# Optimization experiments

Measured on AMD Instinct MI355X. Metric: run time of the kernel, lower is better.

The kernel has to match this reference:

```python
import jax, jax.numpy as jnp
import numpy as np

N, F, D, K, B, L, E, H = 12288, 128, 128, 3, 64, 256, 393216, 8
DT = 2 * D  # token dim
ALPHA = 0.5


def _mlp(h, w1, b1, w2, b2):
    return jax.nn.relu(h @ w1 + b1) @ w2 + b2


def setup_inputs() -> dict:
    key = jax.random.key(0)
    ks = jax.random.split(key, 24)
    s = 0.05
    x = jax.random.normal(ks[0], (N, F), jnp.float32)
    proj_w = jax.random.normal(ks[1], (F, D), jnp.float32) * s
    proj_b = jnp.zeros((D,), jnp.float32)
    adj_rows = jax.random.randint(ks[2], (E,), 0, N, jnp.int32)
    adj_cols = jax.random.randint(ks[3], (E,), 0, N, jnp.int32)
    adj_vals = jax.random.uniform(ks[4], (E,), jnp.float32) / 32.0
    ppr = jax.random.uniform(ks[5], (N, N), jnp.float32) * 0.01
    drnl = jax.random.uniform(ks[6], (B, N), jnp.float32) * 10.0
    src = jax.random.randint(ks[7], (B,), 0, N, jnp.int32)
    dst = jax.random.randint(ks[8], (B,), 0, N, jnp.int32)
    sample_idx = jnp.repeat(jnp.arange(B, dtype=jnp.int32), L)
    node_idx = jax.random.randint(ks[9], (B, L), 0, N, jnp.int32)
    node_idx = node_idx.at[:, 0].set(src).at[:, 1].set(dst).reshape(-1)
    enc_w1 = jax.random.normal(ks[10], (4, 2, D), jnp.float32) * 0.2
    enc_b1 = jnp.zeros((4, D), jnp.float32)
    enc_w2 = jax.random.normal(ks[11], (4, D, D), jnp.float32) * s
    enc_b2 = jnp.zeros((4, D), jnp.float32)
    struct_w1 = jax.random.normal(ks[12], (4 * D, D), jnp.float32) * s
    struct_b1 = jnp.zeros((D,), jnp.float32)
    struct_w2 = jax.random.normal(ks[13], (D, D), jnp.float32) * s
    struct_b2 = jnp.zeros((D,), jnp.float32)
    cls_tok = jax.random.normal(ks[14], (DT,), jnp.float32) * s
    wq = jax.random.normal(ks[15], (DT, DT), jnp.float32) * s
    wk = jax.random.normal(ks[16], (DT, DT), jnp.float32) * s
    wv = jax.random.normal(ks[17], (DT, DT), jnp.float32) * s
    wo = jax.random.normal(ks[18], (DT, DT), jnp.float32) * s
    return dict(x=x, proj_w=proj_w, proj_b=proj_b, adj_vals=adj_vals,
                adj_rows=adj_rows, adj_cols=adj_cols, ppr=ppr, drnl=drnl,
                src=src, dst=dst, sample_idx=sample_idx, node_idx=node_idx,
                enc_w1=enc_w1, enc_b1=enc_b1, enc_w2=enc_w2, enc_b2=enc_b2,
                struct_w1=struct_w1, struct_b1=struct_b1, struct_w2=struct_w2,
                struct_b2=struct_b2, cls_tok=cls_tok, wq=wq, wk=wk, wv=wv, wo=wo)


def reference(x, proj_w, proj_b, adj_vals, adj_rows, adj_cols, ppr, drnl,
              src, dst, sample_idx, node_idx,
              enc_w1, enc_b1, enc_w2, enc_b2,
              struct_w1, struct_b1, struct_w2, struct_b2,
              cls_tok, wq, wk, wv, wo):
    # --- re_features: feature_proj + K sparse matmul hops, APPNP-style mix ---
    feats = x @ proj_w + proj_b                      # [N, D]
    h = feats
    for _ in range(K):
        h = jax.ops.segment_sum(adj_vals[:, None] * h[adj_cols], adj_rows,
                                num_segments=N)      # sparse adj @ h
    re_x = h * (1.0 - ALPHA) + feats * ALPHA         # [N, D]

    # --- cal_heuristic: dense ppr row gather + drnl lookup ---
    n = sample_idx.shape[0]
    ppr_a = ppr[src[sample_idx], node_idx]           # [n]
    ppr_b = ppr[dst[sample_idx], node_idx]
    drnl_v = drnl[sample_idx, node_idx]
    heur = jnp.zeros((n, 4, 2), jnp.float32)
    heur = heur.at[:, 2, 0].set(ppr_a).at[:, 2, 1].set(ppr_b)
    heur = heur.at[:, 3, 0].set(drnl_v).at[:, 3, 1].set(drnl_v)

    # --- tokenizer: 4 heuristic MLPs -> structure MLP, concat node feats ---
    enc = jax.vmap(_mlp)(heur.transpose(1, 0, 2), enc_w1, enc_b1, enc_w2, enc_b2)
    struct_in = enc.transpose(1, 0, 2).reshape(n, 4 * D)   # [n, 4D] (CN,AA,PPR,DRNL)
    struct = _mlp(struct_in, struct_w1, struct_b1, struct_w2, struct_b2)  # [n, D]
    tok = jnp.concatenate([struct, re_x[node_idx]], axis=-1).reshape(B, L, DT)

    # --- GraphTransformer: CLS + multi-head self-attention ---
    cls = jnp.broadcast_to(cls_tok, (B, 1, DT))
    seq = jnp.concatenate([cls, tok], axis=1)        # [B, L+1, DT]
    dh = DT // H
    q = (seq @ wq).reshape(B, L + 1, H, dh)
    k = (seq @ wk).reshape(B, L + 1, H, dh)
    v = (seq @ wv).reshape(B, L + 1, H, dh)
    att = jax.nn.softmax(jnp.einsum('bqhd,bkhd->bhqk', q, k) / jnp.sqrt(jnp.float32(dh)), axis=-1)
    out = jnp.einsum('bhqk,bkhd->bqhd', att, v).reshape(B, L + 1, DT) @ wo
    h_cls, h_a, h_b = out[:, 0], out[:, 1], out[:, 2]
    return jnp.concatenate([h_a, h_b, h_cls], axis=-1)  # [B, 6*dim]
```

## Files before the change

kernel.cpp:

```cpp
#include <hip/hip_runtime.h>
#include <math.h>

#define NN 12288
#define FD 128
#define DD 128
#define EE 393216
#define BB 64
#define LL 256
#define HH 8
#define DTD 256
#define NTOK 16384
#define CAP 128

#define PROJ_B0 1536
#define PREP_B0 1728
#define HEUR_B0 1796
#define SBIAS_B 1860
#define CLS_B   1861
#define SETUP_GRID 1862

#define SEQ_ST 272
#define STG_ST 272

typedef float f32x4 __attribute__((ext_vector_type(4)));
typedef short s16x8 __attribute__((ext_vector_type(8)));

__device__ __forceinline__ float relu_(float x){ return fmaxf(x, 0.0f); }

__device__ __forceinline__ unsigned short f2b(float f){
  unsigned int u = __float_as_uint(f);
  u += 0x7FFFu + ((u >> 16) & 1u);
  return (unsigned short)(u >> 16);
}
__device__ __forceinline__ float b2f(unsigned short h){
  return __uint_as_float(((unsigned int)h) << 16);
}

__device__ __forceinline__ f32x4 MF(s16x8 a, s16x8 b, f32x4 c){
  return __builtin_amdgcn_mfma_f32_16x16x32_bf16(a, b, c, 0, 0, 0);
}

__global__ void __launch_bounds__(256)
k_setup(const float* __restrict__ x, const float* __restrict__ proj_w,
        const float* __restrict__ proj_b, unsigned short* __restrict__ featsb,
        const float* __restrict__ wq, const float* __restrict__ wk,
        const float* __restrict__ wv,
        const float* __restrict__ enc_w2, const float* __restrict__ sw1,
        const float* __restrict__ sw2, const float* __restrict__ cls_tok,
        unsigned short* __restrict__ wqT, unsigned short* __restrict__ wkT,
        unsigned short* __restrict__ wvT,
        unsigned short* __restrict__ w2T2, unsigned short* __restrict__ w2T3,
        unsigned short* __restrict__ sw1aT, unsigned short* __restrict__ sw1bT,
        unsigned short* __restrict__ sw2T,
        const int* __restrict__ node_idx, const int* __restrict__ srcI,
        const int* __restrict__ dstI, const float* __restrict__ ppr,
        const float* __restrict__ drnl, float* __restrict__ heurA,
        float* __restrict__ heurB, float* __restrict__ heurD,
        const int* __restrict__ adj_rows, const int* __restrict__ adj_cols,
        const float* __restrict__ adj_vals, int* __restrict__ cnt,
        uint2* __restrict__ ccv,
        const float* __restrict__ enc_b1, const float* __restrict__ enc_b2,
        const float* __restrict__ sb1, float* __restrict__ sbias,
        float* __restrict__ qcls, unsigned short* __restrict__ kcls,
        unsigned short* __restrict__ vcls){
  int t = threadIdx.x;
  if(blockIdx.x < PROJ_B0){
    int e = blockIdx.x*256 + t;
    int r = adj_rows[e];
    int p = atomicAdd(&cnt[r], 1);
    ccv[(size_t)r*CAP + p] = make_uint2((unsigned)adj_cols[e], __float_as_uint(adj_vals[e]));
  } else if(blockIdx.x < PREP_B0){
    int bid = blockIdx.x - PROJ_B0;
    int row0 = bid * 64;
    int lane = t & 63, w = t >> 6;
    int lr = lane & 15, lg = lane >> 4;
    f32x4 acc[4][2];
    #pragma unroll
    for(int nt=0;nt<2;++nt){
      int col = w*32 + nt*16 + lr;
      float bv = proj_b[col];
      #pragma unroll
      for(int rt=0;rt<4;++rt)
        #pragma unroll
        for(int i=0;i<4;++i) acc[rt][nt][i]=bv;
    }
    #pragma unroll
    for(int ks=0; ks<4; ++ks){
      int kb = ks*32 + lg*8;
      s16x8 Bf[2];
      #pragma unroll
      for(int nt=0;nt<2;++nt){
        int col = w*32 + nt*16 + lr;
        #pragma unroll
        for(int i=0;i<8;++i) Bf[nt][i] = (short)f2b(proj_w[(kb+i)*DD + col]);
      }
      #pragma unroll
      for(int rt=0;rt<4;++rt){
        int row = row0 + rt*16 + lr;
        const f32x4* xp = (const f32x4*)(x + (size_t)row*FD + kb);
        f32x4 v0 = xp[0], v1 = xp[1];
        s16x8 Af;
        #pragma unroll
        for(int i=0;i<4;++i){ Af[i] = (short)f2b(v0[i]); Af[4+i] = (short)f2b(v1[i]); }
        #pragma unroll
        for(int nt=0;nt<2;++nt) acc[rt][nt] = MF(Af, Bf[nt], acc[rt][nt]);
      }
    }
    #pragma unroll
    for(int rt=0;rt<4;++rt)
      #pragma unroll
      for(int nt=0;nt<2;++nt)
        #pragma unroll
        for(int i=0;i<4;++i){
          int row = row0 + rt*16 + lg*4 + i;
          int col = w*32 + nt*16 + lr;
          featsb[(size_t)row*DD + col] = f2b(acc[rt][nt][i]);
        }
  } else if(blockIdx.x < HEUR_B0){
    int bid = blockIdx.x - PREP_B0;
    const float* s; unsigned short* d; int S, k0, n0;
    if(bid < 48){
      int m = bid >> 4, t16 = bid & 15;
      s = (m==0)? wq : (m==1)? wk : wv;
      d = (m==0)? wqT : (m==1)? wkT : wvT;
      S = 256; k0 = (t16>>2)*64; n0 = (t16&3)*64;
    } else {
      int b2 = bid - 48; int m = b2 >> 2, t4 = b2 & 3;
      if(m==0){ s = enc_w2 + 2*16384; d = w2T2; }
      else if(m==1){ s = enc_w2 + 3*16384; d = w2T3; }
      else if(m==2){ s = sw1 + 256*128; d = sw1aT; }
      else if(m==3){ s = sw1 + 384*128; d = sw1bT; }
      else { s = sw2; d = sw2T; }
      S = 128; k0 = (t4>>1)*64; n0 = (t4&1)*64;
    }
    __shared__ unsigned short tile[64][65];
    #pragma unroll
    for(int it=0; it<16; ++it){
      int idx = t + it*256;
      int i = idx>>6, j = idx&63;
      tile[i][j] = f2b(s[(size_t)(k0+i)*S + n0 + j]);
    }
    __syncthreads();
    #pragma unroll
    for(int it=0; it<16; ++it){
      int idx = t + it*256;
      int i2 = idx>>6, j2 = idx&63;
      d[(size_t)(n0+i2)*S + k0 + j2] = tile[j2][i2];
    }
  } else if(blockIdx.x < SBIAS_B){
    int tt = (blockIdx.x - HEUR_B0)*256 + t;
    int s = tt >> 8;
    int node = node_idx[tt];
    heurA[tt] = ppr[(size_t)srcI[s]*NN + node];
    heurB[tt] = ppr[(size_t)dstI[s]*NN + node];
    heurD[tt] = drnl[(size_t)s*NN + node];
  } else if(blockIdx.x == SBIAS_B){
    __shared__ float h0[DD], h1[DD], e0[DD], e1[DD];
    if(t < DD){
      h0[t] = relu_(enc_b1[0*DD+t]);
      h1[t] = relu_(enc_b1[1*DD+t]);
    }
    __syncthreads();
    if(t < DD){
      float a0 = enc_b2[0*DD+t], a1 = enc_b2[1*DD+t];
      for(int d2=0; d2<DD; ++d2){
        a0 += h0[d2]*enc_w2[(0*DD+d2)*DD + t];
        a1 += h1[d2]*enc_w2[(1*DD+d2)*DD + t];
      }
      e0[t]=a0; e1[t]=a1;
    }
    __syncthreads();
    if(t < DD){
      float sv = sb1[t];
      for(int d2=0; d2<DD; ++d2)
        sv += e0[d2]*sw1[d2*DD + t] + e1[d2]*sw1[(DD+d2)*DD + t];
      sbias[t]=sv;
    }
  } else {
    __shared__ float scls[DTD];
    scls[t] = cls_tok[t];
    __syncthreads();
    float aq=0.f, ak=0.f, av=0.f;
    for(int d2=0; d2<DTD; ++d2){
      float cv = scls[d2];
      aq += cv*wq[d2*DTD + t];
      ak += cv*wk[d2*DTD + t];
      av += cv*wv[d2*DTD + t];
    }
    qcls[t] = aq;
    kcls[t] = f2b(ak);
    vcls[t] = f2b(av);
  }
}

__global__ void __launch_bounds__(256)
k_spmm_w(const unsigned int* __restrict__ hin32, unsigned int* __restrict__ hout32,
         const int* __restrict__ cnt, const uint2* __restrict__ ccv,
         const unsigned int* __restrict__ featsb32, int finalpass){
  int lane = threadIdx.x & 63;
  int r = blockIdx.x*4 + (threadIdx.x>>6);
  int deg = cnt[r];
  const uint2* base = ccv + (size_t)r*CAP;
  float a0=0.f,a1=0.f,b0=0.f,b1=0.f,c0=0.f,c1=0.f,d0=0.f,d1=0.f;
  int p = 0;
  for(; p+4 <= deg; p += 4){
    uint2 q0 = base[p], q1 = base[p+1], q2 = base[p+2], q3 = base[p+3];
    unsigned u0 = hin32[(size_t)q0.x*64 + lane];
    unsigned u1 = hin32[(size_t)q1.x*64 + lane];
    unsigned u2 = hin32[(size_t)q2.x*64 + lane];
    unsigned u3 = hin32[(size_t)q3.x*64 + lane];
    float v0=__uint_as_float(q0.y), v1=__uint_as_float(q1.y);
    float v2=__uint_as_float(q2.y), v3=__uint_as_float(q3.y);
    a0 += v0*b2f((unsigned short)(u0&0xffffu)); a1 += v0*b2f((unsigned short)(u0>>16));
    b0 += v1*b2f((unsigned short)(u1&0xffffu)); b1 += v1*b2f((unsigned short)(u1>>16));
    c0 += v2*b2f((unsigned short)(u2&0xffffu)); c1 += v2*b2f((unsigned short)(u2>>16));
    d0 += v3*b2f((unsigned short)(u3&0xffffu)); d1 += v3*b2f((unsigned short)(u3>>16));
  }
  for(; p < deg; ++p){
    uint2 q0 = base[p];
    unsigned u0 = hin32[(size_t)q0.x*64 + lane];
    float v0 = __uint_as_float(q0.y);
    a0 += v0*b2f((unsigned short)(u0&0xffffu)); a1 += v0*b2f((unsigned short)(u0>>16));
  }
  a0 += b0 + c0 + d0;
  a1 += b1 + c1 + d1;
  if(finalpass){
    unsigned f = featsb32[(size_t)r*64 + lane];
    a0 = 0.5f*a0 + 0.5f*b2f((unsigned short)(f & 0xffffu));
    a1 = 0.5f*a1 + 0.5f*b2f((unsigned short)(f >> 16));
  }
  hout32[(size_t)r*64 + lane] = (unsigned)f2b(a0) | ((unsigned)f2b(a1) << 16);
}

__global__ void __launch_bounds__(512)
k_tok_kv(const int* __restrict__ node_idx,
         const float* __restrict__ heurA, const float* __restrict__ heurB,
         const float* __restrict__ heurD,
         const float* __restrict__ enc_w1, const float* __restrict__ enc_b1,
         const unsigned short* __restrict__ w2T2, const unsigned short* __restrict__ w2T3,
         const float* __restrict__ enc_b2,
         const unsigned short* __restrict__ sw1aT, const unsigned short* __restrict__ sw1bT,
         const float* __restrict__ sbias,
         const unsigned short* __restrict__ sw2T, const float* __restrict__ sb2,
         const unsigned short* __restrict__ rexb,
         const unsigned short* __restrict__ wkT, const unsigned short* __restrict__ wvT,
         const unsigned short* __restrict__ wqT,
         unsigned short* __restrict__ kbuf, unsigned short* __restrict__ vbuf,
         float* __restrict__ qbuf){
  __shared__ float sA[64], sB[64], sDV[64];
  __shared__ int sNode[64];
  __shared__ __align__(16) unsigned short hid[64*136];
  __shared__ __align__(16) unsigned short uni[64*STG_ST];
  unsigned short* pe2 = uni;
  unsigned short* pe3 = uni + 64*136;
  unsigned short* seq = uni;
  unsigned short* stg = uni;

  int tid = threadIdx.x;
  int lane = tid & 63;
  int w = tid >> 6;
  int lr = lane & 15;
  int lg = lane >> 4;
  int t0 = blockIdx.x * 64;
  int bs = t0 >> 8;
  int p0 = t0 & 255;

  if(tid < 64){
    int tt = t0 + tid;
    sNode[tid] = node_idx[tt];
    sA[tid]  = heurA[tt];
    sB[tid]  = heurB[tt];
    sDV[tid] = heurD[tt];
  }
  __syncthreads();

  int colm = w*16 + lr;

  {
    f32x4 acc2[4], acc3[4];
    float b2v = enc_b2[2*DD + colm];
    float b3v = enc_b2[3*DD + colm];
    #pragma unroll
    for(int rt=0;rt<4;++rt)
      #pragma unroll
      for(int i=0;i<4;++i){ acc2[rt][i]=b2v; acc3[rt][i]=b3v; }
    #pragma unroll
    for(int ks=0; ks<4; ++ks){
      int kb = ks*32 + lg*8;
      float w20[8], w21[8], w3s[8], b2c[8], b3c[8];
      #pragma unroll
      for(int i=0;i<8;++i){
        int k = kb + i;
        w20[i] = enc_w1[4*DD + k];
        w21[i] = enc_w1[5*DD + k];
        w3s[i] = enc_w1[6*DD + k] + enc_w1[7*DD + k];
        b2c[i] = enc_b1[2*DD + k];
        b3c[i] = enc_b1[3*DD + k];
      }
      s16x8 B2 = *(const s16x8*)(w2T2 + colm*DD + kb);
      s16x8 B3 = *(const s16x8*)(w2T3 + colm*DD + kb);
      #pragma unroll
      for(int rt=0;rt<4;++rt){
        int row = rt*16 + lr;
        float a = sA[row], b = sB[row], dv = sDV[row];
        s16x8 A2, A3;
        #pragma unroll
        for(int i=0;i<8;++i){
          A2[i] = (short)f2b(relu_(a*w20[i] + b*w21[i] + b2c[i]));
          A3[i] = (short)f2b(relu_(dv*w3s[i] + b3c[i]));
        }
        acc2[rt] = MF(A2, B2, acc2[rt]);
        acc3[rt] = MF(A3, B3, acc3[rt]);
      }
    }
    #pragma unroll
    for(int rt=0;rt<4;++rt)
      #pragma unroll
      for(int i=0;i<4;++i){
        int row = rt*16 + lg*4 + i;
        pe2[row*136 + colm] = f2b(acc2[rt][i]);
        pe3[row*136 + colm] = f2b(acc3[rt][i]);
      }
  }
  __syncthreads();

  {
    f32x4 acc[4];
    float sv = sbias[colm];
    #pragma unroll
    for(int rt=0;rt<4;++rt)
      #pragma unroll
      for(int i=0;i<4;++i) acc[rt][i]=sv;
    #pragma unroll
    for(int ks=0; ks<4; ++ks){
      int kb = ks*32 + lg*8;
      s16x8 Ba = *(const s16x8*)(sw1aT + colm*DD + kb);
      s16x8 Bb = *(const s16x8*)(sw1bT + colm*DD + kb);
      #pragma unroll
      for(int rt=0;rt<4;++rt){
        s16x8 A2 = *(const s16x8*)&pe2[(rt*16+lr)*136 + kb];
        s16x8 A3 = *(const s16x8*)&pe3[(rt*16+lr)*136 + kb];
        acc[rt] = MF(A2, Ba, acc[rt]);
        acc[rt] = MF(A3, Bb, acc[rt]);
      }
    }
    __syncthreads();
    #pragma unroll
    for(int rt=0;rt<4;++rt)
      #pragma unroll
      for(int i=0;i<4;++i){
        int row = rt*16 + lg*4 + i;
        hid[row*136 + colm] = f2b(relu_(acc[rt][i]));
      }
  }
  __syncthreads();

  {
    f32x4 acc[4];
    float bv = sb2[colm];
    #pragma unroll
    for(int rt=0;rt<4;++rt)
      #pragma unroll
      for(int i=0;i<4;++i) acc[rt][i]=bv;
    #pragma unroll
    for(int ks=0; ks<4; ++ks){
      int kb = ks*32 + lg*8;
      s16x8 Bc = *(const s16x8*)(sw2T + colm*DD + kb);
      #pragma unroll
      for(int rt=0;rt<4;++rt){
        s16x8 A = *(const s16x8*)&hid[(rt*16+lr)*136 + kb];
        acc[rt] = MF(A, Bc, acc[rt]);
      }
    }
    #pragma unroll
    for(int rt=0;rt<4;++rt)
      #pragma unroll
      for(int i=0;i<4;++i){
        int row = rt*16 + lg*4 + i;
        seq[row*SEQ_ST + colm] = f2b(acc[rt][i]);
      }
    int row = tid >> 3, c = (tid & 7)*16;
    int node = sNode[row];
    const unsigned short* rp = rexb + (size_t)node*DD + c;
    *(s16x8*)(seq + row*SEQ_ST + DD + c)     = *(const s16x8*)(rp);
    *(s16x8*)(seq + row*SEQ_ST + DD + c + 8) = *(const s16x8*)(rp + 8);
  }
  __syncthreads();

  f32x4 accK[4][2], accV[4][2];
  {
    #pragma unroll
    for(int rt=0;rt<4;++rt)
      #pragma unroll
      for(int nt=0;nt<2;++nt)
        #pragma unroll
        for(int i=0;i<4;++i){ accK[rt][nt][i]=0.f; accV[rt][nt][i]=0.f; }
    int col0 = w * 32;
    #pragma unroll
    for(int ks=0; ks<8; ++ks){
      int kb = ks*32 + lg*8;
      s16x8 A[4], Bk[2], Bv[2];
      #pragma unroll
      for(int rt=0;rt<4;++rt)
        A[rt] = *(const s16x8*)&seq[(rt*16+lr)*SEQ_ST + kb];
      #pragma unroll
      for(int nt=0;nt<2;++nt){
        int col = col0 + nt*16 + lr;
        Bk[nt] = *(const s16x8*)(wkT + (size_t)col*DTD + kb);
        Bv[nt] = *(const s16x8*)(wvT + (size_t)col*DTD + kb);
      }
      #pragma unroll
      for(int rt=0;rt<4;++rt)
        #pragma unroll
        for(int nt=0;nt<2;++nt){
          accK[rt][nt] = MF(A[rt], Bk[nt], accK[rt][nt]);
          accV[rt][nt] = MF(A[rt], Bv[nt], accV[rt][nt]);
        }
    }
  }
  if(p0 == 0){
    int qi = tid >> 8, col = tid & 255;
    float acc = 0.f;
    for(int d=0; d<DTD; d+=8){
      s16x8 wv8 = *(const s16x8*)(wqT + (size_t)col*DTD + d);
      #pragma unroll
      for(int j=0;j<8;++j)
        acc += b2f(seq[qi*SEQ_ST + d + j]) * b2f((unsigned short)wv8[j]);
    }
    qbuf[(size_t)(bs*2+qi)*DTD + col] = acc;
  }
  __syncthreads();

  {
    int col0 = w * 32;
    #pragma unroll
    for(int rt=0;rt<4;++rt)
      #pragma unroll
      for(int nt=0;nt<2;++nt)
        #pragma unroll
        for(int i=0;i<4;++i)
          stg[(rt*16 + lg*4 + i)*STG_ST + col0 + nt*16 + lr] = f2b(accK[rt][nt][i]);
  }
  __syncthreads();
  {
    int row = tid >> 3, c = (tid & 7)*32;
    #pragma unroll
    for(int j=0;j<4;++j)
      *(s16x8*)(kbuf + (size_t)(t0+row)*DTD + c + j*8) = *(const s16x8*)&stg[row*STG_ST + c + j*8];
  }
  __syncthreads();
  {
    int col0 = w * 32;
    #pragma unroll
    for(int rt=0;rt<4;++rt)
      #pragma unroll
      for(int nt=0;nt<2;++nt)
        #pragma unroll
        for(int i=0;i<4;++i)
          stg[(rt*16 + lg*4 + i)*STG_ST + col0 + nt*16 + lr] = f2b(accV[rt][nt][i]);
  }
  __syncthreads();
  {
    int row = tid >> 3, c = (tid & 7)*32;
    #pragma unroll
    for(int j=0;j<4;++j)
      *(s16x8*)(vbuf + (size_t)(t0+row)*DTD + c + j*8) = *(const s16x8*)&stg[row*STG_ST + c + j*8];
  }
}

__global__ void __launch_bounds__(256)
k_att2(const float* __restrict__ qcls, const float* __restrict__ qbuf,
       const unsigned short* __restrict__ kcls, const unsigned short* __restrict__ vcls,
       const unsigned short* __restrict__ kbuf, const unsigned short* __restrict__ vbuf,
       float* __restrict__ att_o){
  __shared__ float q_s[3][32];
  __shared__ float sc[3][257];
  __shared__ float ppv[8][3][32];
  int t = threadIdx.x;
  int b = blockIdx.x >> 3, h = blockIdx.x & 7;

  if(t < 96){
    int qi = t>>5, dd = t&31;
    q_s[qi][dd] = (qi==0) ? qcls[h*32 + dd]
                          : qbuf[(size_t)(b*2+qi-1)*DTD + h*32 + dd];
  }
  __syncthreads();
  const float scale = 0.17677669529663687f;
  for(int kk=t; kk<257; kk+=256){
    const unsigned short* kr = (kk==0) ? (kcls + h*32)
                                       : (kbuf + (size_t)(b*256+kk-1)*DTD + h*32);
    float kv[32];
    #pragma unroll
    for(int j=0;j<4;++j){
      s16x8 u = *(const s16x8*)(kr + j*8);
      #pragma unroll
      for(int m2=0;m2<8;++m2) kv[j*8+m2] = b2f((unsigned short)u[m2]);
    }
    float d0=0.f,d1=0.f,d2=0.f;
    #pragma unroll
    for(int dd=0;dd<32;++dd){
      d0 += q_s[0][dd]*kv[dd]; d1 += q_s[1][dd]*kv[dd]; d2 += q_s[2][dd]*kv[dd];
    }
    sc[0][kk]=d0*scale; sc[1][kk]=d1*scale; sc[2][kk]=d2*scale;
  }
  __syncthreads();
  {
    int wv = t>>6, lane = t&63;
    if(wv < 3){
      int qi = wv;
      float x0=sc[qi][lane], x1=sc[qi][lane+64], x2=sc[qi][lane+128], x3=sc[qi][lane+192];
      float x4 = (lane==0)? sc[qi][256] : -1e30f;
      float m = fmaxf(fmaxf(fmaxf(x0,x1),fmaxf(x2,x3)),x4);
      #pragma unroll
      for(int off=32; off>0; off>>=1) m = fmaxf(m, __shfl_xor(m, off));
      float e0=expf(x0-m), e1=expf(x1-m), e2v=expf(x2-m), e3v=expf(x3-m);
      float e4=(lane==0)? expf(x4-m) : 0.f;
      float s = e0+e1+e2v+e3v+e4;
      #pragma unroll
      for(int off=32; off>0; off>>=1) s += __shfl_xor(s, off);
      float inv = 1.0f/s;
      sc[qi][lane]=e0*inv; sc[qi][lane+64]=e1*inv;
      sc[qi][lane+128]=e2v*inv; sc[qi][lane+192]=e3v*inv;
      if(lane==0) sc[qi][256]=e4*inv;
    }
  }
  __syncthreads();
  {
    int dd = t & 31, g = t >> 5;
    float a0=0.f, a1=0.f, a2=0.f;
    for(int kk=g; kk<257; kk+=8){
      const unsigned short* vr = (kk==0) ? (vcls + h*32)
                                         : (vbuf + (size_t)(b*256+kk-1)*DTD + h*32);
      float v = b2f(vr[dd]);
      a0 += sc[0][kk]*v; a1 += sc[1][kk]*v; a2 += sc[2][kk]*v;
    }
    ppv[g][0][dd]=a0; ppv[g][1][dd]=a1; ppv[g][2][dd]=a2;
  }
  __syncthreads();
  if(t < 96){
    int qi = t>>5, dd = t&31;
    float s = 0.f;
    #pragma unroll
    for(int gg=0; gg<8; ++gg) s += ppv[gg][qi][dd];
    att_o[(size_t)(b*3+qi)*DTD + h*32 + dd] = s;
  }
}

__global__ void k_out(const float* __restrict__ att_o, const float* __restrict__ wo,
                      float* __restrict__ out){
  __shared__ float srow[DTD];
  int t = threadIdx.x;
  int r = blockIdx.x;
  int b = r/3, qi = r - b*3;
  srow[t] = att_o[(size_t)r*DTD + t];
  __syncthreads();
  float acc = 0.f;
  for(int d=0; d<DTD; ++d) acc += srow[d]*wo[d*DTD + t];
  int off = (qi==1)? 0 : ((qi==2)? DTD : 2*DTD);
  out[(size_t)b*768 + off + t] = acc;
}

extern "C" void kernel_launch(void* const* d_in, const int* in_sizes, int n_in,
                              void* d_out, int out_size, void* d_ws, size_t ws_size,
                              hipStream_t stream){
  const float* x        = (const float*)d_in[0];
  const float* proj_w   = (const float*)d_in[1];
  const float* proj_b   = (const float*)d_in[2];
  const float* adj_vals = (const float*)d_in[3];
  const int*   adj_rows = (const int*)d_in[4];
  const int*   adj_cols = (const int*)d_in[5];
  const float* ppr      = (const float*)d_in[6];
  const float* drnl     = (const float*)d_in[7];
  const int*   srcI     = (const int*)d_in[8];
  const int*   dstI     = (const int*)d_in[9];
  const int*   node_idx   = (const int*)d_in[11];
  const float* enc_w1   = (const float*)d_in[12];
  const float* enc_b1   = (const float*)d_in[13];
  const float* enc_w2   = (const float*)d_in[14];
  const float* enc_b2   = (const float*)d_in[15];
  const float* sw1      = (const float*)d_in[16];
  const float* sb1      = (const float*)d_in[17];
  const float* sw2      = (const float*)d_in[18];
  const float* sb2      = (const float*)d_in[19];
  const float* cls_tok  = (const float*)d_in[20];
  const float* wq       = (const float*)d_in[21];
  const float* wk       = (const float*)d_in[22];
  const float* wv       = (const float*)d_in[23];
  const float* wo       = (const float*)d_in[24];
  float* out = (float*)d_out;

  char* p = (char*)d_ws;
  auto alloc = [&](size_t bytes)->void*{ void* r = (void*)p; p += (bytes + 63) & ~(size_t)63; return r; };
  unsigned short* featsb = (unsigned short*)alloc((size_t)NN*DD*2);
  unsigned short* h1b    = (unsigned short*)alloc((size_t)NN*DD*2);
  unsigned short* h2b    = (unsigned short*)alloc((size_t)NN*DD*2);
  unsigned short* rexb   = (unsigned short*)alloc((size_t)NN*DD*2);
  int*   cnt     = (int*)  alloc((size_t)NN*4);
  uint2* ccv     = (uint2*)alloc((size_t)NN*CAP*8);
  float* sbias   = (float*)alloc((size_t)DD*4);
  float* heurA   = (float*)alloc((size_t)NTOK*4);
  float* heurB   = (float*)alloc((size_t)NTOK*4);
  float* heurD   = (float*)alloc((size_t)NTOK*4);
  unsigned short* kbuf = (unsigned short*)alloc((size_t)NTOK*DTD*2);
  unsigned short* vbuf = (unsigned short*)alloc((size_t)NTOK*DTD*2);
  float* qbuf    = (float*)alloc((size_t)BB*2*DTD*4);
  float* qcls    = (float*)alloc((size_t)DTD*4);
  unsigned short* kcls = (unsigned short*)alloc((size_t)DTD*2);
  unsigned short* vcls = (unsigned short*)alloc((size_t)DTD*2);
  float* att_o   = (float*)alloc((size_t)BB*3*DTD*4);
  unsigned short* wqT   = (unsigned short*)alloc((size_t)DTD*DTD*2);
  unsigned short* wkT   = (unsigned short*)alloc((size_t)DTD*DTD*2);
  unsigned short* wvT   = (unsigned short*)alloc((size_t)DTD*DTD*2);
  unsigned short* w2T2  = (unsigned short*)alloc((size_t)DD*DD*2);
  unsigned short* w2T3  = (unsigned short*)alloc((size_t)DD*DD*2);
  unsigned short* sw1aT = (unsigned short*)alloc((size_t)DD*DD*2);
  unsigned short* sw1bT = (unsigned short*)alloc((size_t)DD*DD*2);
  unsigned short* sw2T  = (unsigned short*)alloc((size_t)DD*DD*2);

  hipMemsetAsync(cnt, 0, NN*sizeof(int), stream);

  k_setup  <<<SETUP_GRID, 256, 0, stream>>>(x, proj_w, proj_b, featsb,
                                            wq, wk, wv, enc_w2, sw1, sw2, cls_tok,
                                            wqT, wkT, wvT, w2T2, w2T3, sw1aT, sw1bT, sw2T,
                                            node_idx, srcI, dstI, ppr, drnl,
                                            heurA, heurB, heurD,
                                            adj_rows, adj_cols, adj_vals, cnt, ccv,
                                            enc_b1, enc_b2, sb1, sbias,
                                            qcls, kcls, vcls);
  k_spmm_w <<<NN/4,   256, 0, stream>>>((const unsigned*)featsb, (unsigned*)h1b, cnt, ccv, (const unsigned*)featsb, 0);
  k_spmm_w <<<NN/4,   256, 0, stream>>>((const unsigned*)h1b, (unsigned*)h2b, cnt, ccv, (const unsigned*)featsb, 0);
  k_spmm_w <<<NN/4,   256, 0, stream>>>((const unsigned*)h2b, (unsigned*)rexb, cnt, ccv, (const unsigned*)featsb, 1);
  k_tok_kv <<<NTOK/64,512, 0, stream>>>(node_idx, heurA, heurB, heurD,
                                        enc_w1, enc_b1, w2T2, w2T3, enc_b2,
                                        sw1aT, sw1bT, sbias, sw2T, sb2, rexb,
                                        wkT, wvT, wqT, kbuf, vbuf, qbuf);
  k_att2   <<<BB*HH,  256, 0, stream>>>(qcls, qbuf, kcls, vcls, kbuf, vbuf, att_o);
  k_out    <<<BB*3,   256, 0, stream>>>(att_o, wo, out);
}
```

Before: 154.2 us.

## Fuse adjacency scatter and three SpMM passes into one cooperative kernel; fuse attention with output projection

Moves the adjacency bucketing out of the setup kernel and runs it, together with the counter zeroing and the three propagation passes, inside a single cooperative kernel that uses grid-wide syncs between phases. This replaces a memset and four separate launches. It also merges the per-head attention kernel and the output-projection kernel into one kernel per (batch, query) that handles all heads, removing the att_o round trip. Risks are grid-sync cost and lower occupancy with only 1024 persistent blocks on the SpMM phase, and fewer blocks (192) in the attention kernel. If the cooperative launch fails, the code falls back to separate kernels.

```diff
diff --git a/kernel.cpp b/kernel.cpp
--- a/kernel.cpp
+++ b/kernel.cpp
@@ -1,4 +1,5 @@
 #include <hip/hip_runtime.h>
+#include <hip/hip_cooperative_groups.h>
 #include <math.h>
 
 #define NN 12288
@@ -12,12 +13,14 @@
 #define NTOK 16384
 #define CAP 128
 
-#define PROJ_B0 1536
-#define PREP_B0 1728
-#define HEUR_B0 1796
-#define SBIAS_B 1860
-#define CLS_B   1861
-#define SETUP_GRID 1862
+#define PROJ_B0 0
+#define PREP_B0 192
+#define HEUR_B0 260
+#define SBIAS_B 324
+#define CLS_B   325
+#define SETUP_GRID 326
+
+#define COOP_BLOCKS 1024
 
 #define SEQ_ST 272
 #define STG_ST 272
@@ -38,6 +41,91 @@
 
 __device__ __forceinline__ f32x4 MF(s16x8 a, s16x8 b, f32x4 c){
   return __builtin_amdgcn_mfma_f32_16x16x32_bf16(a, b, c, 0, 0, 0);
+}
+
+__device__ __forceinline__ void spmm_row(int r, int lane,
+    const unsigned int* __restrict__ hin32, unsigned int* __restrict__ hout32,
+    const int* __restrict__ cnt, const uint2* __restrict__ ccv,
+    const unsigned int* __restrict__ featsb32, int finalpass){
+  int deg = cnt[r];
+  const uint2* base = ccv + (size_t)r*CAP;
+  float a0=0.f,a1=0.f,b0=0.f,b1=0.f,c0=0.f,c1=0.f,d0=0.f,d1=0.f;
+  int p = 0;
+  for(; p+4 <= deg; p += 4){
+    uint2 q0 = base[p], q1 = base[p+1], q2 = base[p+2], q3 = base[p+3];
+    unsigned u0 = hin32[(size_t)q0.x*64 + lane];
+    unsigned u1 = hin32[(size_t)q1.x*64 + lane];
+    unsigned u2 = hin32[(size_t)q2.x*64 + lane];
+    unsigned u3 = hin32[(size_t)q3.x*64 + lane];
+    float v0=__uint_as_float(q0.y), v1=__uint_as_float(q1.y);
+    float v2=__uint_as_float(q2.y), v3=__uint_as_float(q3.y);
+    a0 += v0*b2f((unsigned short)(u0&0xffffu)); a1 += v0*b2f((unsigned short)(u0>>16));
+    b0 += v1*b2f((unsigned short)(u1&0xffffu)); b1 += v1*b2f((unsigned short)(u1>>16));
+    c0 += v2*b2f((unsigned short)(u2&0xffffu)); c1 += v2*b2f((unsigned short)(u2>>16));
+    d0 += v3*b2f((unsigned short)(u3&0xffffu)); d1 += v3*b2f((unsigned short)(u3>>16));
+  }
+  for(; p < deg; ++p){
+    uint2 q0 = base[p];
+    unsigned u0 = hin32[(size_t)q0.x*64 + lane];
+    float v0 = __uint_as_float(q0.y);
+    a0 += v0*b2f((unsigned short)(u0&0xffffu)); a1 += v0*b2f((unsigned short)(u0>>16));
+  }
+  a0 += b0 + c0 + d0;
+  a1 += b1 + c1 + d1;
+  if(finalpass){
+    unsigned f = featsb32[(size_t)r*64 + lane];
+    a0 = 0.5f*a0 + 0.5f*b2f((unsigned short)(f & 0xffffu));
+    a1 = 0.5f*a1 + 0.5f*b2f((unsigned short)(f >> 16));
+  }
+  hout32[(size_t)r*64 + lane] = (unsigned)f2b(a0) | ((unsigned)f2b(a1) << 16);
+}
+
+__global__ void __launch_bounds__(256, 4)
+k_coop(unsigned short* __restrict__ featsb, unsigned short* __restrict__ h1b,
+       unsigned short* __restrict__ h2b, unsigned short* __restrict__ rexb,
+       int* __restrict__ cnt, uint2* __restrict__ ccv,
+       const int* __restrict__ adj_rows, const int* __restrict__ adj_cols,
+       const float* __restrict__ adj_vals){
+  cooperative_groups::grid_group gg = cooperative_groups::this_grid();
+  int t = threadIdx.x, bid = blockIdx.x;
+  int gid = bid*256 + t;
+  int lane = t & 63, wv = t >> 6;
+
+  if(gid < NN) cnt[gid] = 0;
+  gg.sync();
+
+  for(int e = gid; e < EE; e += COOP_BLOCKS*256){
+    int r = adj_rows[e];
+    int p = atomicAdd(&cnt[r], 1);
+    ccv[(size_t)r*CAP + p] = make_uint2((unsigned)adj_cols[e], __float_as_uint(adj_vals[e]));
+  }
+  gg.sync();
+
+  int r0 = bid*12 + wv*3;
+  #pragma unroll
+  for(int i=0;i<3;++i) spmm_row(r0+i, lane, (const unsigned*)featsb, (unsigned*)h1b, cnt, ccv, (const unsigned*)featsb, 0);
+  gg.sync();
+  #pragma unroll
+  for(int i=0;i<3;++i) spmm_row(r0+i, lane, (const unsigned*)h1b, (unsigned*)h2b, cnt, ccv, (const unsigned*)featsb, 0);
+  gg.sync();
+  #pragma unroll
+  for(int i=0;i<3;++i) spmm_row(r0+i, lane, (const unsigned*)h2b, (unsigned*)rexb, cnt, ccv, (const unsigned*)featsb, 1);
+}
+
+__global__ void k_scatter(const int* __restrict__ rows, const int* __restrict__ cols,
+                          const float* __restrict__ vals, int* __restrict__ cnt,
+                          uint2* __restrict__ ccv){
+  int e = blockIdx.x*256 + threadIdx.x;
+  int r = rows[e];
+  int p = atomicAdd(&cnt[r], 1);
+  ccv[(size_t)r*CAP + p] = make_uint2((unsigned)cols[e], __float_as_uint(vals[e]));
+}
+__global__ void __launch_bounds__(256)
+k_spmm_w(const unsigned int* __restrict__ hin32, unsigned int* __restrict__ hout32,
+         const int* __restrict__ cnt, const uint2* __restrict__ ccv,
+         const unsigned int* __restrict__ featsb32, int finalpass){
+  spmm_row(blockIdx.x*4 + (threadIdx.x>>6), threadIdx.x & 63,
+           hin32, hout32, cnt, ccv, featsb32, finalpass);
 }
 
 __global__ void __launch_bounds__(256)
@@ -56,20 +144,12 @@
         const int* __restrict__ dstI, const float* __restrict__ ppr,
         const float* __restrict__ drnl, float* __restrict__ heurA,
         float* __restrict__ heurB, float* __restrict__ heurD,
-        const int* __restrict__ adj_rows, const int* __restrict__ adj_cols,
-        const float* __restrict__ adj_vals, int* __restrict__ cnt,
-        uint2* __restrict__ ccv,
         const float* __restrict__ enc_b1, const float* __restrict__ enc_b2,
         const float* __restrict__ sb1, float* __restrict__ sbias,
         float* __restrict__ qcls, unsigned short* __restrict__ kcls,
         unsigned short* __restrict__ vcls){
   int t = threadIdx.x;
-  if(blockIdx.x < PROJ_B0){
-    int e = blockIdx.x*256 + t;
-    int r = adj_rows[e];
-    int p = atomicAdd(&cnt[r], 1);
-    ccv[(size_t)r*CAP + p] = make_uint2((unsigned)adj_cols[e], __float_as_uint(adj_vals[e]));
-  } else if(blockIdx.x < PREP_B0){
+  if(blockIdx.x < PREP_B0){
     int bid = blockIdx.x - PROJ_B0;
     int row0 = bid * 64;
     int lane = t & 63, w = t >> 6;
@@ -191,45 +271,6 @@
     kcls[t] = f2b(ak);
     vcls[t] = f2b(av);
   }
-}
-
-__global__ void __launch_bounds__(256)
-k_spmm_w(const unsigned int* __restrict__ hin32, unsigned int* __restrict__ hout32,
-         const int* __restrict__ cnt, const uint2* __restrict__ ccv,
-         const unsigned int* __restrict__ featsb32, int finalpass){
-  int lane = threadIdx.x & 63;
-  int r = blockIdx.x*4 + (threadIdx.x>>6);
-  int deg = cnt[r];
-  const uint2* base = ccv + (size_t)r*CAP;
-  float a0=0.f,a1=0.f,b0=0.f,b1=0.f,c0=0.f,c1=0.f,d0=0.f,d1=0.f;
-  int p = 0;
-  for(; p+4 <= deg; p += 4){
-    uint2 q0 = base[p], q1 = base[p+1], q2 = base[p+2], q3 = base[p+3];
-    unsigned u0 = hin32[(size_t)q0.x*64 + lane];
-    unsigned u1 = hin32[(size_t)q1.x*64 + lane];
-    unsigned u2 = hin32[(size_t)q2.x*64 + lane];
-    unsigned u3 = hin32[(size_t)q3.x*64 + lane];
-    float v0=__uint_as_float(q0.y), v1=__uint_as_float(q1.y);
-    float v2=__uint_as_float(q2.y), v3=__uint_as_float(q3.y);
-    a0 += v0*b2f((unsigned short)(u0&0xffffu)); a1 += v0*b2f((unsigned short)(u0>>16));
-    b0 += v1*b2f((unsigned short)(u1&0xffffu)); b1 += v1*b2f((unsigned short)(u1>>16));
-    c0 += v2*b2f((unsigned short)(u2&0xffffu)); c1 += v2*b2f((unsigned short)(u2>>16));
-    d0 += v3*b2f((unsigned short)(u3&0xffffu)); d1 += v3*b2f((unsigned short)(u3>>16));
-  }
-  for(; p < deg; ++p){
-    uint2 q0 = base[p];
-    unsigned u0 = hin32[(size_t)q0.x*64 + lane];
-    float v0 = __uint_as_float(q0.y);
-    a0 += v0*b2f((unsigned short)(u0&0xffffu)); a1 += v0*b2f((unsigned short)(u0>>16));
-  }
-  a0 += b0 + c0 + d0;
-  a1 += b1 + c1 + d1;
-  if(finalpass){
-    unsigned f = featsb32[(size_t)r*64 + lane];
-    a0 = 0.5f*a0 + 0.5f*b2f((unsigned short)(f & 0xffffu));
-    a1 = 0.5f*a1 + 0.5f*b2f((unsigned short)(f >> 16));
-  }
-  hout32[(size_t)r*64 + lane] = (unsigned)f2b(a0) | ((unsigned)f2b(a1) << 16);
 }
 
 __global__ void __launch_bounds__(512)
@@ -469,47 +510,43 @@
 }
 
 __global__ void __launch_bounds__(256)
-k_att2(const float* __restrict__ qcls, const float* __restrict__ qbuf,
-       const unsigned short* __restrict__ kcls, const unsigned short* __restrict__ vcls,
-       const unsigned short* __restrict__ kbuf, const unsigned short* __restrict__ vbuf,
-       float* __restrict__ att_o){
-  __shared__ float q_s[3][32];
-  __shared__ float sc[3][257];
-  __shared__ float ppv[8][3][32];
+k_att_out(const float* __restrict__ qcls, const float* __restrict__ qbuf,
+          const unsigned short* __restrict__ kcls, const unsigned short* __restrict__ vcls,
+          const unsigned short* __restrict__ kbuf, const unsigned short* __restrict__ vbuf,
+          const float* __restrict__ wo, float* __restrict__ out){
+  __shared__ float q_s[DTD];
+  __shared__ float sc[HH][257];
+  __shared__ float ao[DTD];
   int t = threadIdx.x;
-  int b = blockIdx.x >> 3, h = blockIdx.x & 7;
-
-  if(t < 96){
-    int qi = t>>5, dd = t&31;
-    q_s[qi][dd] = (qi==0) ? qcls[h*32 + dd]
-                          : qbuf[(size_t)(b*2+qi-1)*DTD + h*32 + dd];
-  }
+  int b = blockIdx.x / 3, qi = blockIdx.x - b*3;
+
+  q_s[t] = (qi==0) ? qcls[t] : qbuf[(size_t)(b*2+qi-1)*DTD + t];
   __syncthreads();
   const float scale = 0.17677669529663687f;
   for(int kk=t; kk<257; kk+=256){
-    const unsigned short* kr = (kk==0) ? (kcls + h*32)
-                                       : (kbuf + (size_t)(b*256+kk-1)*DTD + h*32);
-    float kv[32];
-    #pragma unroll
-    for(int j=0;j<4;++j){
+    const unsigned short* kr = (kk==0) ? kcls : (kbuf + (size_t)(b*256+kk-1)*DTD);
+    float acc[HH];
+    #pragma unroll
+    for(int h=0;h<HH;++h) acc[h]=0.f;
+    #pragma unroll
+    for(int j=0;j<32;++j){
       s16x8 u = *(const s16x8*)(kr + j*8);
-      #pragma unroll
-      for(int m2=0;m2<8;++m2) kv[j*8+m2] = b2f((unsigned short)u[m2]);
-    }
-    float d0=0.f,d1=0.f,d2=0.f;
-    #pragma unroll
-    for(int dd=0;dd<32;++dd){
-      d0 += q_s[0][dd]*kv[dd]; d1 += q_s[1][dd]*kv[dd]; d2 += q_s[2][dd]*kv[dd];
-    }
-    sc[0][kk]=d0*scale; sc[1][kk]=d1*scale; sc[2][kk]=d2*scale;
+      float p = 0.f;
+      #pragma unroll
+      for(int m=0;m<8;++m) p += q_s[j*8+m]*b2f((unsigned short)u[m]);
+      acc[j>>2] += p;
+    }
+    #pragma unroll
+    for(int h=0;h<HH;++h) sc[h][kk] = acc[h]*scale;
   }
   __syncthreads();
   {
     int wv = t>>6, lane = t&63;
-    if(wv < 3){
-      int qi = wv;
-      float x0=sc[qi][lane], x1=sc[qi][lane+64], x2=sc[qi][lane+128], x3=sc[qi][lane+192];
-      float x4 = (lane==0)? sc[qi][256] : -1e30f;
+    #pragma unroll
+    for(int j=0;j<2;++j){
+      int h = wv*2 + j;
+      float x0=sc[h][lane], x1=sc[h][lane+64], x2=sc[h][lane+128], x3=sc[h][lane+192];
+      float x4 = (lane==0)? sc[h][256] : -1e30f;
       float m = fmaxf(fmaxf(fmaxf(x0,x1),fmaxf(x2,x3)),x4);
       #pragma unroll
       for(int off=32; off>0; off>>=1) m = fmaxf(m, __shfl_xor(m, off));
@@ -519,45 +556,32 @@
       #pragma unroll
       for(int off=32; off>0; off>>=1) s += __shfl_xor(s, off);
       float inv = 1.0f/s;
-      sc[qi][lane]=e0*inv; sc[qi][lane+64]=e1*inv;
-      sc[qi][lane+128]=e2v*inv; sc[qi][lane+192]=e3v*inv;
-      if(lane==0) sc[qi][256]=e4*inv;
-    }
-  }
-  __syncthreads();
-  {
-    int dd = t & 31, g = t >> 5;
-    float a0=0.f, a1=0.f, a2=0.f;
-    for(int kk=g; kk<257; kk+=8){
-      const unsigned short* vr = (kk==0) ? (vcls + h*32)
-                                         : (vbuf + (size_t)(b*256+kk-1)*DTD + h*32);
-      float v = b2f(vr[dd]);
-      a0 += sc[0][kk]*v; a1 += sc[1][kk]*v; a2 += sc[2][kk]*v;
-    }
-    ppv[g][0][dd]=a0; ppv[g][1][dd]=a1; ppv[g][2][dd]=a2;
-  }
-  __syncthreads();
-  if(t < 96){
-    int qi = t>>5, dd = t&31;
-    float s = 0.f;
-    #pragma unroll
-    for(int gg=0; gg<8; ++gg) s += ppv[gg][qi][dd];
-    att_o[(size_t)(b*3+qi)*DTD + h*32 + dd] = s;
-  }
-}
-
-__global__ void k_out(const float* __restrict__ att_o, const float* __restrict__ wo,
-                      float* __restrict__ out){
-  __shared__ float srow[DTD];
-  int t = threadIdx.x;
-  int r = blockIdx.x;
-  int b = r/3, qi = r - b*3;
-  srow[t] = att_o[(size_t)r*DTD + t];
-  __syncthreads();
-  float acc = 0.f;
-  for(int d=0; d<DTD; ++d) acc += srow[d]*wo[d*DTD + t];
-  int off = (qi==1)? 0 : ((qi==2)? DTD : 2*DTD);
-  out[(size_t)b*768 + off + t] = acc;
+      sc[h][lane]=e0*inv; sc[h][lane+64]=e1*inv;
+      sc[h][lane+128]=e2v*inv; sc[h][lane+192]=e3v*inv;
+      if(lane==0) sc[h][256]=e4*inv;
+    }
+  }
+  __syncthreads();
+  {
+    int h = t>>5, dd = t&31;
+    float a0 = sc[h][0]*b2f(vcls[h*32+dd]);
+    float a1=0.f, a2=0.f, a3=0.f;
+    const unsigned short* vb = vbuf + (size_t)b*256*DTD + h*32 + dd;
+    for(int kk=1; kk<257; kk+=4){
+      a0 += sc[h][kk]  *b2f(vb[(size_t)(kk-1)*DTD]);
+      a1 += sc[h][kk+1]*b2f(vb[(size_t)(kk)*DTD]);
+      a2 += sc[h][kk+2]*b2f(vb[(size_t)(kk+1)*DTD]);
+      a3 += sc[h][kk+3]*b2f(vb[(size_t)(kk+2)*DTD]);
+    }
+    ao[t] = a0+a1+a2+a3;
+  }
+  __syncthreads();
+  {
+    float acc = 0.f;
+    for(int d=0; d<DTD; ++d) acc += ao[d]*wo[d*DTD + t];
+    int off = (qi==1)? 0 : ((qi==2)? DTD : 2*DTD);
+    out[(size_t)b*768 + off + t] = acc;
+  }
 }
 
 extern "C" void kernel_launch(void* const* d_in, const int* in_sizes, int n_in,
@@ -607,7 +631,6 @@
   float* qcls    = (float*)alloc((size_t)DTD*4);
   unsigned short* kcls = (unsigned short*)alloc((size_t)DTD*2);
   unsigned short* vcls = (unsigned short*)alloc((size_t)DTD*2);
-  float* att_o   = (float*)alloc((size_t)BB*3*DTD*4);
   unsigned short* wqT   = (unsigned short*)alloc((size_t)DTD*DTD*2);
   unsigned short* wkT   = (unsigned short*)alloc((size_t)DTD*DTD*2);
   unsigned short* wvT   = (unsigned short*)alloc((size_t)DTD*DTD*2);
@@ -617,23 +640,33 @@
   unsigned short* sw1bT = (unsigned short*)alloc((size_t)DD*DD*2);
   unsigned short* sw2T  = (unsigned short*)alloc((size_t)DD*DD*2);
 
-  hipMemsetAsync(cnt, 0, NN*sizeof(int), stream);
-
   k_setup  <<<SETUP_GRID, 256, 0, stream>>>(x, proj_w, proj_b, featsb,
                                             wq, wk, wv, enc_w2, sw1, sw2, cls_tok,
                                             wqT, wkT, wvT, w2T2, w2T3, sw1aT, sw1bT, sw2T,
                                             node_idx, srcI, dstI, ppr, drnl,
                                             heurA, heurB, heurD,
-                                            adj_rows, adj_cols, adj_vals, cnt, ccv,
                                             enc_b1, enc_b2, sb1, sbias,
                                             qcls, kcls, vcls);
-  k_spmm_w <<<NN/4,   256, 0, stream>>>((const unsigned*)featsb, (unsigned*)h1b, cnt, ccv, (const unsigned*)featsb, 0);
-  k_spmm_w <<<NN/4,   256, 0, stream>>>((const unsigned*)h1b, (unsigned*)h2b, cnt, ccv, (const unsigned*)featsb, 0);
-  k_spmm_w <<<NN/4,   256, 0, stream>>>((const unsigned*)h2b, (unsigned*)rexb, cnt, ccv, (const unsigned*)featsb, 1);
-  k_tok_kv <<<NTOK/64,512, 0, stream>>>(node_idx, heurA, heurB, heurD,
-                                        enc_w1, enc_b1, w2T2, w2T3, enc_b2,
-                                        sw1aT, sw1bT, sbias, sw2T, sb2, rexb,
-                                        wkT, wvT, wqT, kbuf, vbuf, qbuf);
-  k_att2   <<<BB*HH,  256, 0, stream>>>(qcls, qbuf, kcls, vcls, kbuf, vbuf, att_o);
-  k_out    <<<BB*3,   256, 0, stream>>>(att_o, wo, out);
-}
+
+  {
+    unsigned short *a0=featsb, *a1=h1b, *a2=h2b, *a3=rexb;
+    int* a4 = cnt; uint2* a5 = ccv;
+    const int* a6 = adj_rows; const int* a7 = adj_cols; const float* a8 = adj_vals;
+    void* args[] = {&a0,&a1,&a2,&a3,&a4,&a5,&a6,&a7,&a8};
+    hipError_t err = hipLaunchCooperativeKernel((const void*)k_coop,
+                       dim3(COOP_BLOCKS), dim3(256), args, 0, stream);
+    if(err != hipSuccess){
+      hipMemsetAsync(cnt, 0, NN*sizeof(int), stream);
+      k_scatter<<<EE/256, 256, 0, stream>>>(adj_rows, adj_cols, adj_vals, cnt, ccv);
+      k_spmm_w <<<NN/4,   256, 0, stream>>>((const unsigned*)featsb, (unsigned*)h1b, cnt, ccv, (const unsigned*)featsb, 0);
+      k_spmm_w <<<NN/4,   256, 0, stream>>>((const unsigned*)h1b, (unsigned*)h2b, cnt, ccv, (const unsigned*)featsb, 0);
+      k_spmm_w <<<NN/4,   256, 0, stream>>>((const unsigned*)h2b, (unsigned*)rexb, cnt, ccv, (const unsigned*)featsb, 1);
+    }
+  }
+
+  k_tok_kv <<<NTOK/64, 512, 0, stream>>>(node_idx, heurA, heurB, heurD,
+                                         enc_w1, enc_b1, w2T2, w2T3, enc_b2,
+                                         sw1aT, sw1bT, sbias, sw2T, sb2, rexb,
+                                         wkT, wvT, wqT, kbuf, vbuf, qbuf);
+  k_att_out<<<BB*3,    256, 0, stream>>>(qcls, qbuf, kcls, vcls, kbuf, vbuf, wo, out);
+}
```

After: 581.7 us. +277.3%, slower.
